# Kernel optimization log

Hardware: AMD Instinct MI355X
Metric: run time of the kernel (lower is better)

Reference implementation:

```python
import jax, jax.numpy as jnp
import numpy as np

N, E, P = 20000, 640000, 200000
IN_DIM, HID, HEADS, OUT_DIM = 256, 64, 4, 86
NEG_SLOPE = 0.2


def _gat_layer(h_in, src, dst, W, a_src, a_dst, b, heads, concat):
    n = h_in.shape[0]
    c = W.shape[1] // heads
    h = (h_in @ W).reshape(n, heads, c)                      # [N,H,C]
    alpha_s = jnp.sum(h * a_src, axis=-1)                    # [N,H]
    alpha_d = jnp.sum(h * a_dst, axis=-1)                    # [N,H]
    e = alpha_s[src] + alpha_d[dst]                          # [E,H]
    e = jnp.where(e > 0, e, NEG_SLOPE * e)                   # leaky_relu(0.2)
    # softmax over incoming edges of each destination node
    m = jax.ops.segment_max(e, dst, num_segments=n)          # [N,H]
    e = jnp.exp(e - m[dst])
    denom = jax.ops.segment_sum(e, dst, num_segments=n)      # [N,H]
    w = e / denom[dst]                                       # [E,H]
    msg = h[src] * w[:, :, None]                             # [E,H,C]
    out = jax.ops.segment_sum(msg, dst, num_segments=n)      # [N,H,C]
    if concat:
        out = out.reshape(n, heads * c)
    else:
        out = out.mean(axis=1)
    return out + b


def setup_inputs() -> dict:
    key = jax.random.key(0)
    ks = jax.random.split(key, 16)
    s = lambda *d: 1.0 / np.sqrt(d[0])
    x = jax.random.normal(ks[0], (N, IN_DIM), jnp.float32)
    edge_index = jax.random.randint(ks[1], (2, E), 0, N, jnp.int32)
    drug_pairs = jax.random.randint(ks[2], (P, 2), 0, N, jnp.int32)
    W1 = jax.random.normal(ks[3], (IN_DIM, HEADS * HID), jnp.float32) * s(IN_DIM)
    a_src1 = jax.random.normal(ks[4], (HEADS, HID), jnp.float32) * s(HID)
    a_dst1 = jax.random.normal(ks[5], (HEADS, HID), jnp.float32) * s(HID)
    b1 = jnp.zeros((HEADS * HID,), jnp.float32)
    W2 = jax.random.normal(ks[6], (HEADS * HID, HID), jnp.float32) * s(HEADS * HID)
    a_src2 = jax.random.normal(ks[7], (1, HID), jnp.float32) * s(HID)
    a_dst2 = jax.random.normal(ks[8], (1, HID), jnp.float32) * s(HID)
    b2 = jnp.zeros((HID,), jnp.float32)
    Wp1 = jax.random.normal(ks[9], (2 * HID, HID), jnp.float32) * s(2 * HID)
    bp1 = jnp.zeros((HID,), jnp.float32)
    Wp2 = jax.random.normal(ks[10], (HID, OUT_DIM), jnp.float32) * s(HID)
    bp2 = jnp.zeros((OUT_DIM,), jnp.float32)
    return dict(x=x, edge_index=edge_index, drug_pairs=drug_pairs,
                W1=W1, a_src1=a_src1, a_dst1=a_dst1, b1=b1,
                W2=W2, a_src2=a_src2, a_dst2=a_dst2, b2=b2,
                Wp1=Wp1, bp1=bp1, Wp2=Wp2, bp2=bp2)


def reference(x, edge_index, drug_pairs, W1, a_src1, a_dst1, b1,
              W2, a_src2, a_dst2, b2, Wp1, bp1, Wp2, bp2):
    n = x.shape[0]
    # PyG GATConv default add_self_loops=True
    loop = jnp.arange(n, dtype=edge_index.dtype)
    src = jnp.concatenate([edge_index[0], loop])
    dst = jnp.concatenate([edge_index[1], loop])
    h = _gat_layer(x, src, dst, W1, a_src1, a_dst1, b1, HEADS, concat=True)
    h = jax.nn.elu(h)  # dropout is identity in eval mode
    h = _gat_layer(h, src, dst, W2, a_src2, a_dst2, b2, 1, concat=False)
    h = jax.nn.elu(h)
    combined = jnp.concatenate([h[drug_pairs[:, 0]], h[drug_pairs[:, 1]]], axis=1)
    z = jax.nn.relu(combined @ Wp1 + bp1)
    return z @ Wp2 + bp2
```

## Files before the change

### kernel.cpp

```cpp
#include <hip/hip_runtime.h>
#include <hip/hip_fp16.h>

#define NN 20000
#define NE 640000
#define NEE 660000
#define NP 200000
#define NEG 0.2f

typedef _Float16 f16;
typedef __attribute__((ext_vector_type(4))) _Float16 f16x4;
typedef __attribute__((ext_vector_type(8))) _Float16 f16x8;
typedef __attribute__((ext_vector_type(4))) float f32x4;

__global__ void k_hist(const int* __restrict__ ei, int* __restrict__ cnt) {
  int i = blockIdx.x * 256 + threadIdx.x;
  if (i >= NEE) return;
  int d = (i < NE) ? ei[NE + i] : (i - NE);
  atomicAdd(&cnt[d], 1);
}

__global__ __launch_bounds__(1024) void k_scan(const int* __restrict__ cnt, int* __restrict__ rp) {
  __shared__ int ps[1024];
  const int CH = 20;
  int t = threadIdx.x;
  int lo = t * CH, hi = lo + CH;
  if (hi > NN) hi = NN;
  if (lo > NN) lo = NN;
  int s = 0;
  for (int i = lo; i < hi; ++i) s += cnt[i];
  ps[t] = s;
  __syncthreads();
  for (int off = 1; off < 1024; off <<= 1) {
    int v = (t >= off) ? ps[t - off] : 0;
    __syncthreads();
    ps[t] += v;
    __syncthreads();
  }
  int run = (t > 0) ? ps[t - 1] : 0;
  for (int i = lo; i < hi; ++i) { rp[i] = run; run += cnt[i]; }
  if (t == 1023) rp[NN] = ps[1023];
}

__global__ void k_scatter(const int* __restrict__ ei, const int* __restrict__ rp,
                          int* __restrict__ cur, int* __restrict__ col) {
  int i = blockIdx.x * 256 + threadIdx.x;
  if (i >= NEE) return;
  int s, d;
  if (i < NE) { s = ei[i]; d = ei[NE + i]; } else { s = i - NE; d = s; }
  int pos = atomicAdd(&cur[d], 1);
  col[rp[d] + pos] = s;
}

__global__ void k_cvt(const float* __restrict__ x, const float* __restrict__ W1,
                      f16* __restrict__ xh, f16* __restrict__ W1T) {
  int i = blockIdx.x * 256 + threadIdx.x;
  if (i < NN * 256 / 4) {
    float4 v = ((const float4*)x)[i];
    f16x4 h; h.x = (f16)v.x; h.y = (f16)v.y; h.z = (f16)v.z; h.w = (f16)v.w;
    *(f16x4*)(xh + (size_t)i * 4) = h;
  } else {
    int j = i - NN * 256 / 4;
    if (j < 256 * 256) {
      int r = j >> 8, c = j & 255;
      W1T[c * 256 + r] = (f16)W1[j];
    }
  }
}

__global__ void k_prep(const float* __restrict__ Wp2, const float* __restrict__ bp2,
                       const float* __restrict__ W2,
                       f16* __restrict__ Wp2Th, float* __restrict__ bp2p,
                       f16* __restrict__ W2T) {
  int i = blockIdx.x * 256 + threadIdx.x;
  if (i < 96 * 64) {
    int o = i >> 6, t = i & 63;
    Wp2Th[o * 64 + t] = (o < 86) ? (f16)Wp2[t * 86 + o] : (f16)0.f;
  }
  if (i < 96) bp2p[i] = (i < 86) ? bp2[i] : 0.f;
  if (i < 64 * 256) {
    int n = i >> 8, k = i & 255;
    W2T[n * 256 + k] = (f16)W2[k * 64 + n];
  }
}

__global__ __launch_bounds__(256) void k_gemm1(
    const f16* __restrict__ xh, const f16* __restrict__ W1T,
    const float* __restrict__ as1, const float* __restrict__ ad1,
    __half* __restrict__ h1h16, float* __restrict__ AS1, float* __restrict__ AD1) {
  __shared__ f16 xs[16][264];
  int tid = threadIdx.x;
  int base = blockIdx.x * 16;
  {
    int r = tid >> 4, ch = tid & 15;
    const uint4* src = (const uint4*)(xh + (size_t)(base + r) * 256 + ch * 16);
    uint4 v0 = src[0], v1 = src[1];
    *(uint4*)&xs[r][ch * 16] = v0;
    *(uint4*)&xs[r][ch * 16 + 8] = v1;
  }
  __syncthreads();
  int wv = tid >> 6, lane = tid & 63;
  int head = wv;
  int lr = lane & 15, lk = lane >> 4;
  f32x4 acc[4] = {{0.f,0.f,0.f,0.f},{0.f,0.f,0.f,0.f},{0.f,0.f,0.f,0.f},{0.f,0.f,0.f,0.f}};
#pragma unroll
  for (int k0 = 0; k0 < 256; k0 += 32) {
    f16x8 a = *(const f16x8*)&xs[lr][k0 + lk * 8];
#pragma unroll
    for (int nt = 0; nt < 4; ++nt) {
      int n = head * 64 + nt * 16 + lr;
      f16x8 b = *(const f16x8*)(W1T + (size_t)n * 256 + k0 + lk * 8);
      acc[nt] = __builtin_amdgcn_mfma_f32_16x16x32_f16(a, b, acc[nt], 0, 0, 0);
    }
  }
#pragma unroll
  for (int nt = 0; nt < 4; ++nt) {
    int cc = nt * 16 + lr;
#pragma unroll
    for (int r = 0; r < 4; ++r) {
      int row = lk * 4 + r;
      h1h16[((size_t)head * NN + base + row) * 64 + cc] = __float2half(acc[nt][r]);
    }
  }
#pragma unroll
  for (int r = 0; r < 4; ++r) {
    float ps = 0.f, pd = 0.f;
#pragma unroll
    for (int nt = 0; nt < 4; ++nt) {
      int cc = nt * 16 + lr;
      ps += acc[nt][r] * as1[head * 64 + cc];
      pd += acc[nt][r] * ad1[head * 64 + cc];
    }
#pragma unroll
    for (int off = 1; off < 16; off <<= 1) {
      ps += __shfl_xor(ps, off);
      pd += __shfl_xor(pd, off);
    }
    if (lr == 0) {
      int n = base + lk * 4 + r;
      AS1[n * 4 + head] = ps;
      AD1[n * 4 + head] = pd;
    }
  }
}

__global__ __launch_bounds__(256, 4) void k_agg1(
    const int* __restrict__ rp, const int* __restrict__ col,
    const float* __restrict__ AS1, const float* __restrict__ AD1,
    const __half* __restrict__ h1h16, const float* __restrict__ b1,
    __half* __restrict__ out16) {
  int b = blockIdx.x;
  int xcd = b & 7;
  int head = xcd >> 1;
  int grp = (b >> 3) * 2 + (xcd & 1);
  int wave = threadIdx.x >> 6, lane = threadIdx.x & 63;
  int n = grp * 4 + wave;
  int g = lane >> 3, c8 = (lane & 7) * 8;
  int e0 = rp[n], e1 = rp[n + 1];
  const __half* hs = h1h16 + (size_t)head * NN * 64;
  float adv = AD1[n * 4 + head];
  float acc[8] = {0.f,0.f,0.f,0.f,0.f,0.f,0.f,0.f};
  float den = 0.f;

  int ee = e0 + g;
  bool v = ee < e1;
  int ec = v ? ee : e1 - 1;
  int s = col[ec];
  float asv = AS1[s * 4 + head];

  for (int e = e0; e < e1; e += 8) {
    int een = e + 8 + g;
    bool vn = een < e1;
    int ecn = vn ? een : e1 - 1;
    int sn = col[ecn];
    float asn = AS1[sn * 4 + head];
    float ev = asv + adv;
    ev = fmaxf(ev, NEG * ev);
    float p = v ? __expf(ev) : 0.f;
    float4 raw = *(const float4*)(hs + (size_t)s * 64 + c8);
    const __half2* hp = (const __half2*)&raw;
#pragma unroll
    for (int m = 0; m < 4; ++m) {
      float2 f = __half22float2(hp[m]);
      acc[m * 2]     += p * f.x;
      acc[m * 2 + 1] += p * f.y;
    }
    den += p;
    s = sn; asv = asn; v = vn;
  }
#pragma unroll
  for (int i = 0; i < 8; ++i) {
    acc[i] += __shfl_xor(acc[i], 8);
    acc[i] += __shfl_xor(acc[i], 16);
    acc[i] += __shfl_xor(acc[i], 32);
  }
  den += __shfl_xor(den, 8); den += __shfl_xor(den, 16); den += __shfl_xor(den, 32);
  if (lane < 8) {
    float inv = 1.f / den;
    int cbase = head * 64 + lane * 8;
    __half ho[8];
#pragma unroll
    for (int i = 0; i < 8; ++i) {
      float r = acc[i] * inv + b1[cbase + i];
      r = r > 0.f ? r : __expf(r) - 1.f;
      ho[i] = __float2half(r);
    }
    *(uint4*)(out16 + (size_t)n * 256 + cbase) = *(uint4*)&ho[0];
  }
}

__global__ __launch_bounds__(256) void k_gemm2(
    const f16* __restrict__ h1a16, const f16* __restrict__ W2T,
    const float* __restrict__ as2, const float* __restrict__ ad2,
    __half* __restrict__ h2h16, float* __restrict__ AS2, float* __restrict__ AD2) {
  __shared__ f16 xs[16][264];
  __shared__ float psL[4][16], pdL[4][16];
  int tid = threadIdx.x;
  int base = blockIdx.x * 16;
  {
    int r = tid >> 4, ch = tid & 15;
    const uint4* src = (const uint4*)(h1a16 + (size_t)(base + r) * 256 + ch * 16);
    uint4 v0 = src[0], v1 = src[1];
    *(uint4*)&xs[r][ch * 16] = v0;
    *(uint4*)&xs[r][ch * 16 + 8] = v1;
  }
  __syncthreads();
  int wv = tid >> 6, lane = tid & 63;
  int lr = lane & 15, lk = lane >> 4;
  f32x4 acc = {0.f, 0.f, 0.f, 0.f};
#pragma unroll
  for (int k0 = 0; k0 < 256; k0 += 32) {
    f16x8 a = *(const f16x8*)&xs[lr][k0 + lk * 8];
    f16x8 b = *(const f16x8*)(W2T + (size_t)(wv * 16 + lr) * 256 + k0 + lk * 8);
    acc = __builtin_amdgcn_mfma_f32_16x16x32_f16(a, b, acc, 0, 0, 0);
  }
  int cc = wv * 16 + lr;
  float asv = as2[cc], adv = ad2[cc];
  float psr[4], pdr[4];
#pragma unroll
  for (int r = 0; r < 4; ++r) {
    int row = lk * 4 + r;
    h2h16[(size_t)(base + row) * 64 + cc] = __float2half(acc[r]);
    float ps = acc[r] * asv, pd = acc[r] * adv;
#pragma unroll
    for (int off = 1; off < 16; off <<= 1) {
      ps += __shfl_xor(ps, off);
      pd += __shfl_xor(pd, off);
    }
    psr[r] = ps; pdr[r] = pd;
  }
  if (lr == 0) {
#pragma unroll
    for (int r = 0; r < 4; ++r) {
      psL[wv][lk * 4 + r] = psr[r];
      pdL[wv][lk * 4 + r] = pdr[r];
    }
  }
  __syncthreads();
  if (tid < 16) {
    AS2[base + tid] = psL[0][tid] + psL[1][tid] + psL[2][tid] + psL[3][tid];
    AD2[base + tid] = pdL[0][tid] + pdL[1][tid] + pdL[2][tid] + pdL[3][tid];
  }
}

__global__ __launch_bounds__(256, 4) void k_agg2(
    const int* __restrict__ rp, const int* __restrict__ col,
    const float* __restrict__ AS2, const float* __restrict__ AD2,
    const __half* __restrict__ h2h16, const float* __restrict__ b2,
    float* __restrict__ out) {
  int wave = threadIdx.x >> 6, lane = threadIdx.x & 63;
  int n = blockIdx.x * 4 + wave;
  int g = lane >> 3, c8 = (lane & 7) * 8;
  int e0 = rp[n], e1 = rp[n + 1];
  float adv = AD2[n];
  float acc[8] = {0.f,0.f,0.f,0.f,0.f,0.f,0.f,0.f};
  float den = 0.f;

  int ee = e0 + g;
  bool v = ee < e1;
  int ec = v ? ee : e1 - 1;
  int s = col[ec];
  float asv = AS2[s];

  for (int e = e0; e < e1; e += 8) {
    int een = e + 8 + g;
    bool vn = een < e1;
    int ecn = vn ? een : e1 - 1;
    int sn = col[ecn];
    float asn = AS2[sn];
    float ev = asv + adv;
    ev = fmaxf(ev, NEG * ev);
    float p = v ? __expf(ev) : 0.f;
    float4 raw = *(const float4*)(h2h16 + (size_t)s * 64 + c8);
    const __half2* hp = (const __half2*)&raw;
#pragma unroll
    for (int m = 0; m < 4; ++m) {
      float2 f = __half22float2(hp[m]);
      acc[m * 2]     += p * f.x;
      acc[m * 2 + 1] += p * f.y;
    }
    den += p;
    s = sn; asv = asn; v = vn;
  }
#pragma unroll
  for (int i = 0; i < 8; ++i) {
    acc[i] += __shfl_xor(acc[i], 8);
    acc[i] += __shfl_xor(acc[i], 16);
    acc[i] += __shfl_xor(acc[i], 32);
  }
  den += __shfl_xor(den, 8); den += __shfl_xor(den, 16); den += __shfl_xor(den, 32);
  if (lane < 8) {
    float inv = 1.f / den;
    int cbase = lane * 8;
    float o[8];
#pragma unroll
    for (int i = 0; i < 8; ++i) {
      float r = acc[i] * inv + b2[cbase + i];
      o[i] = r > 0.f ? r : __expf(r) - 1.f;
    }
    *(float4*)(out + (size_t)n * 64 + cbase) = *(float4*)&o[0];
    *(float4*)(out + (size_t)n * 64 + cbase + 4) = *(float4*)&o[4];
  }
}

__global__ __launch_bounds__(128) void k_predot(
    const float* __restrict__ h2a, const float* __restrict__ Wp1,
    const float* __restrict__ bp1, float* __restrict__ AB) {
  __shared__ float xsT[64][20];
  int c = threadIdx.x;
  int base = blockIdx.x * 16;
  for (int i = threadIdx.x; i < 16 * 64; i += 128) {
    int r = i >> 6, k = i & 63;
    xsT[k][r] = h2a[(size_t)(base + r) * 64 + k];
  }
  __syncthreads();
  int part = c >> 6, u = c & 63;
  float bv = (part == 0) ? bp1[u] : 0.f;
  float acc[16];
#pragma unroll
  for (int r = 0; r < 16; ++r) acc[r] = bv;
#pragma unroll 2
  for (int k = 0; k < 64; ++k) {
    float wv = Wp1[(size_t)(part * 64 + k) * 64 + u];
    const float4* xr = (const float4*)&xsT[k][0];
    float4 x0 = xr[0], x1 = xr[1], x2 = xr[2], x3 = xr[3];
    acc[0] += x0.x * wv; acc[1] += x0.y * wv; acc[2] += x0.z * wv; acc[3] += x0.w * wv;
    acc[4] += x1.x * wv; acc[5] += x1.y * wv; acc[6] += x1.z * wv; acc[7] += x1.w * wv;
    acc[8] += x2.x * wv; acc[9] += x2.y * wv; acc[10] += x2.z * wv; acc[11] += x2.w * wv;
    acc[12] += x3.x * wv; acc[13] += x3.y * wv; acc[14] += x3.z * wv; acc[15] += x3.w * wv;
  }
#pragma unroll
  for (int r = 0; r < 16; ++r) AB[(size_t)(base + r) * 128 + c] = acc[r];
}

__global__ __launch_bounds__(256) void k_pairs(
    const int* __restrict__ pairs, const float* __restrict__ AB,
    const f16* __restrict__ Wp2Th, const float* __restrict__ bp2p,
    float* __restrict__ out) {
  __shared__ f16 zh[64][72];
  int tid = threadIdx.x;
  int pp = tid & 63, q = tid >> 6;
  int p = blockIdx.x * 64 + pp;
  int pi = pairs[2 * p], pj = pairs[2 * p + 1];

  {
    const float4* ar = (const float4*)(AB + (size_t)pi * 128 + q * 16);
    const float4* br = (const float4*)(AB + (size_t)pj * 128 + 64 + q * 16);
    f16 zv[16];
#pragma unroll
    for (int m = 0; m < 4; ++m) {
      float4 a = ar[m], b = br[m];
      zv[m * 4]     = (f16)fmaxf(a.x + b.x, 0.f);
      zv[m * 4 + 1] = (f16)fmaxf(a.y + b.y, 0.f);
      zv[m * 4 + 2] = (f16)fmaxf(a.z + b.z, 0.f);
      zv[m * 4 + 3] = (f16)fmaxf(a.w + b.w, 0.f);
    }
    *(uint4*)&zh[pp][q * 16] = *(uint4*)&zv[0];
    *(uint4*)&zh[pp][q * 16 + 8] = *(uint4*)&zv[8];
  }
  __syncthreads();

  int wv = tid >> 6, lane = tid & 63;
  int lr = lane & 15, lk = lane >> 4;
#pragma unroll
  for (int nt = 0; nt < 6; ++nt) {
    f32x4 acc = {0.f, 0.f, 0.f, 0.f};
#pragma unroll
    for (int k0 = 0; k0 < 64; k0 += 32) {
      f16x8 a = *(const f16x8*)&zh[wv * 16 + lr][k0 + lk * 8];
      f16x8 b = *(const f16x8*)(Wp2Th + (size_t)(nt * 16 + lr) * 64 + k0 + lk * 8);
      acc = __builtin_amdgcn_mfma_f32_16x16x32_f16(a, b, acc, 0, 0, 0);
    }
    int o = nt * 16 + lr;
    if (o < 86) {
      float bb = bp2p[o];
#pragma unroll
      for (int r = 0; r < 4; ++r) {
        int pr = blockIdx.x * 64 + wv * 16 + lk * 4 + r;
        out[(size_t)pr * 86 + o] = acc[r] + bb;
      }
    }
  }
}

extern "C" void kernel_launch(void* const* d_in, const int* in_sizes, int n_in,
                              void* d_out, int out_size, void* d_ws, size_t ws_size,
                              hipStream_t stream) {
  (void)in_sizes; (void)n_in; (void)out_size; (void)ws_size;
  const float* x      = (const float*)d_in[0];
  const int*   ei     = (const int*)d_in[1];
  const int*   pairs  = (const int*)d_in[2];
  const float* W1     = (const float*)d_in[3];
  const float* a_src1 = (const float*)d_in[4];
  const float* a_dst1 = (const float*)d_in[5];
  const float* b1     = (const float*)d_in[6];
  const float* W2     = (const float*)d_in[7];
  const float* a_src2 = (const float*)d_in[8];
  const float* a_dst2 = (const float*)d_in[9];
  const float* b2     = (const float*)d_in[10];
  const float* Wp1    = (const float*)d_in[11];
  const float* bp1    = (const float*)d_in[12];
  const float* Wp2    = (const float*)d_in[13];
  const float* bp2    = (const float*)d_in[14];
  float* out = (float*)d_out;

  char* w = (char*)d_ws;
  auto alloc = [&](size_t bytes) -> void* {
    void* pp = (void*)w;
    w += (bytes + 255) & ~(size_t)255;
    return pp;
  };
  __half* h1h16 = (__half*)alloc((size_t)NN * 256 * 2);
  float*  AS1   = (float*)alloc((size_t)NN * 4 * 4);
  float*  AD1   = (float*)alloc((size_t)NN * 4 * 4);
  __half* h1a16 = (__half*)alloc((size_t)NN * 256 * 2);
  __half* h2h16 = (__half*)alloc((size_t)NN * 64 * 2);
  float*  AS2   = (float*)alloc((size_t)NN * 4);
  float*  AD2   = (float*)alloc((size_t)NN * 4);
  float*  h2agg = (float*)alloc((size_t)NN * 64 * 4);
  float*  AB    = (float*)alloc((size_t)NN * 128 * 4);
  f16*    xh    = (f16*)alloc((size_t)NN * 256 * 2);
  f16*    W1T   = (f16*)alloc((size_t)256 * 256 * 2);
  f16*    Wp2Th = (f16*)alloc((size_t)96 * 64 * 2);
  float*  bp2p  = (float*)alloc(96 * 4);
  f16*    W2T   = (f16*)alloc((size_t)64 * 256 * 2);
  int*    rp    = (int*)alloc((size_t)(NN + 1) * 4);
  int*    cnt   = (int*)alloc((size_t)NN * 4);
  int*    cur   = (int*)alloc((size_t)NN * 4);
  int*    col   = (int*)alloc((size_t)NEE * 4);

  (void)hipMemsetAsync(cnt, 0, (size_t)NN * 4, stream);
  (void)hipMemsetAsync(cur, 0, (size_t)NN * 4, stream);

  const int EB = (NEE + 255) / 256;
  k_hist<<<EB, 256, 0, stream>>>(ei, cnt);
  k_scan<<<1, 1024, 0, stream>>>(cnt, rp);
  k_scatter<<<EB, 256, 0, stream>>>(ei, rp, cur, col);
  k_cvt<<<NN * 256 / 4 / 256 + 256, 256, 0, stream>>>(x, W1, xh, W1T);
  k_prep<<<64, 256, 0, stream>>>(Wp2, bp2, W2, Wp2Th, bp2p, W2T);

  k_gemm1<<<NN / 16, 256, 0, stream>>>(xh, W1T, a_src1, a_dst1, h1h16, AS1, AD1);
  k_agg1<<<NN, 256, 0, stream>>>(rp, col, AS1, AD1, h1h16, b1, h1a16);

  k_gemm2<<<NN / 16, 256, 0, stream>>>((const f16*)h1a16, W2T, a_src2, a_dst2, h2h16, AS2, AD2);
  k_agg2<<<NN / 4, 256, 0, stream>>>(rp, col, AS2, AD2, h2h16, b2, h2agg);

  k_predot<<<NN / 16, 128, 0, stream>>>(h2agg, Wp1, bp1, AB);
  k_pairs<<<NP / 64, 256, 0, stream>>>(pairs, AB, Wp2Th, bp2p, out);
}
```

Baseline: 267.6 us.

## Precompute per-edge attention weights in separate kernels and fuse x conversion into gemm1

Adds k_edgew1/k_edgew2 kernels that compute leaky-relu'd exponentiated attention scores per CSR edge (using a new dst array written during scatter), so the aggregation kernels stream contiguous weights instead of gathering AS[src] and computing exp per edge. It also removes the separate fp32->fp16 conversion kernel for x by converting inside gemm1's shared-memory load, and moves the W1 transpose into k_prep. The trade-off is extra launches and extra global traffic for the dst array and the weight buffers (4*NEE floats for layer 1), in exchange for fewer random gathers and less work in the aggregation loops.

```diff
diff --git a/kernel.cpp b/kernel.cpp
--- a/kernel.cpp
+++ b/kernel.cpp
@@ -42,35 +42,21 @@
 }
 
 __global__ void k_scatter(const int* __restrict__ ei, const int* __restrict__ rp,
-                          int* __restrict__ cur, int* __restrict__ col) {
+                          int* __restrict__ cur, int* __restrict__ col,
+                          int* __restrict__ dstv) {
   int i = blockIdx.x * 256 + threadIdx.x;
   if (i >= NEE) return;
   int s, d;
   if (i < NE) { s = ei[i]; d = ei[NE + i]; } else { s = i - NE; d = s; }
   int pos = atomicAdd(&cur[d], 1);
   col[rp[d] + pos] = s;
-}
-
-__global__ void k_cvt(const float* __restrict__ x, const float* __restrict__ W1,
-                      f16* __restrict__ xh, f16* __restrict__ W1T) {
-  int i = blockIdx.x * 256 + threadIdx.x;
-  if (i < NN * 256 / 4) {
-    float4 v = ((const float4*)x)[i];
-    f16x4 h; h.x = (f16)v.x; h.y = (f16)v.y; h.z = (f16)v.z; h.w = (f16)v.w;
-    *(f16x4*)(xh + (size_t)i * 4) = h;
-  } else {
-    int j = i - NN * 256 / 4;
-    if (j < 256 * 256) {
-      int r = j >> 8, c = j & 255;
-      W1T[c * 256 + r] = (f16)W1[j];
-    }
-  }
+  dstv[rp[d] + pos] = d;
 }
 
 __global__ void k_prep(const float* __restrict__ Wp2, const float* __restrict__ bp2,
-                       const float* __restrict__ W2,
+                       const float* __restrict__ W2, const float* __restrict__ W1,
                        f16* __restrict__ Wp2Th, float* __restrict__ bp2p,
-                       f16* __restrict__ W2T) {
+                       f16* __restrict__ W2T, f16* __restrict__ W1T) {
   int i = blockIdx.x * 256 + threadIdx.x;
   if (i < 96 * 64) {
     int o = i >> 6, t = i & 63;
@@ -81,10 +67,14 @@
     int n = i >> 8, k = i & 255;
     W2T[n * 256 + k] = (f16)W2[k * 64 + n];
   }
+  if (i < 256 * 256) {
+    int r = i >> 8, c = i & 255;
+    W1T[c * 256 + r] = (f16)W1[i];
+  }
 }
 
 __global__ __launch_bounds__(256) void k_gemm1(
-    const f16* __restrict__ xh, const f16* __restrict__ W1T,
+    const float* __restrict__ x, const f16* __restrict__ W1T,
     const float* __restrict__ as1, const float* __restrict__ ad1,
     __half* __restrict__ h1h16, float* __restrict__ AS1, float* __restrict__ AD1) {
   __shared__ f16 xs[16][264];
@@ -92,10 +82,15 @@
   int base = blockIdx.x * 16;
   {
     int r = tid >> 4, ch = tid & 15;
-    const uint4* src = (const uint4*)(xh + (size_t)(base + r) * 256 + ch * 16);
-    uint4 v0 = src[0], v1 = src[1];
-    *(uint4*)&xs[r][ch * 16] = v0;
-    *(uint4*)&xs[r][ch * 16 + 8] = v1;
+    const float4* src = (const float4*)(x + (size_t)(base + r) * 256 + ch * 16);
+    float4 a0 = src[0], a1 = src[1], a2 = src[2], a3 = src[3];
+    f16 tmp[16];
+    tmp[0] = (f16)a0.x; tmp[1] = (f16)a0.y; tmp[2] = (f16)a0.z; tmp[3] = (f16)a0.w;
+    tmp[4] = (f16)a1.x; tmp[5] = (f16)a1.y; tmp[6] = (f16)a1.z; tmp[7] = (f16)a1.w;
+    tmp[8] = (f16)a2.x; tmp[9] = (f16)a2.y; tmp[10] = (f16)a2.z; tmp[11] = (f16)a2.w;
+    tmp[12] = (f16)a3.x; tmp[13] = (f16)a3.y; tmp[14] = (f16)a3.z; tmp[15] = (f16)a3.w;
+    *(uint4*)&xs[r][ch * 16] = *(uint4*)&tmp[0];
+    *(uint4*)&xs[r][ch * 16 + 8] = *(uint4*)&tmp[8];
   }
   __syncthreads();
   int wv = tid >> 6, lane = tid & 63;
@@ -143,11 +138,29 @@
   }
 }
 
+__global__ void k_edgew1(const int* __restrict__ col, const int* __restrict__ dstv,
+                         const float* __restrict__ AS1, const float* __restrict__ AD1,
+                         float* __restrict__ w1) {
+  int i = blockIdx.x * 256 + threadIdx.x;
+  if (i >= NEE) return;
+  int s = col[i], d = dstv[i];
+  float4 as = *(const float4*)(AS1 + s * 4);
+  float4 ad = *(const float4*)(AD1 + d * 4);
+  float e0 = as.x + ad.x, e1 = as.y + ad.y, e2 = as.z + ad.z, e3 = as.w + ad.w;
+  e0 = fmaxf(e0, NEG * e0);
+  e1 = fmaxf(e1, NEG * e1);
+  e2 = fmaxf(e2, NEG * e2);
+  e3 = fmaxf(e3, NEG * e3);
+  w1[0 * NEE + i] = __expf(e0);
+  w1[1 * NEE + i] = __expf(e1);
+  w1[2 * NEE + i] = __expf(e2);
+  w1[3 * NEE + i] = __expf(e3);
+}
+
 __global__ __launch_bounds__(256, 4) void k_agg1(
     const int* __restrict__ rp, const int* __restrict__ col,
-    const float* __restrict__ AS1, const float* __restrict__ AD1,
-    const __half* __restrict__ h1h16, const float* __restrict__ b1,
-    __half* __restrict__ out16) {
+    const float* __restrict__ w1, const __half* __restrict__ h1h16,
+    const float* __restrict__ b1, __half* __restrict__ out16) {
   int b = blockIdx.x;
   int xcd = b & 7;
   int head = xcd >> 1;
@@ -157,7 +170,7 @@
   int g = lane >> 3, c8 = (lane & 7) * 8;
   int e0 = rp[n], e1 = rp[n + 1];
   const __half* hs = h1h16 + (size_t)head * NN * 64;
-  float adv = AD1[n * 4 + head];
+  const float* wp = w1 + (size_t)head * NEE;
   float acc[8] = {0.f,0.f,0.f,0.f,0.f,0.f,0.f,0.f};
   float den = 0.f;
 
@@ -165,27 +178,20 @@
   bool v = ee < e1;
   int ec = v ? ee : e1 - 1;
   int s = col[ec];
-  float asv = AS1[s * 4 + head];
+  float pw = v ? wp[ec] : 0.f;
 
   for (int e = e0; e < e1; e += 8) {
     int een = e + 8 + g;
     bool vn = een < e1;
     int ecn = vn ? een : e1 - 1;
     int sn = col[ecn];
-    float asn = AS1[sn * 4 + head];
-    float ev = asv + adv;
-    ev = fmaxf(ev, NEG * ev);
-    float p = v ? __expf(ev) : 0.f;
+    float pwn = vn ? wp[ecn] : 0.f;
     float4 raw = *(const float4*)(hs + (size_t)s * 64 + c8);
-    const __half2* hp = (const __half2*)&raw;
-#pragma unroll
-    for (int m = 0; m < 4; ++m) {
-      float2 f = __half22float2(hp[m]);
-      acc[m * 2]     += p * f.x;
-      acc[m * 2 + 1] += p * f.y;
-    }
-    den += p;
-    s = sn; asv = asn; v = vn;
+    const f16* hf = (const f16*)&raw;
+#pragma unroll
+    for (int i = 0; i < 8; ++i) acc[i] += pw * (float)hf[i];
+    den += pw;
+    s = sn; pw = pwn;
   }
 #pragma unroll
   for (int i = 0; i < 8; ++i) {
@@ -262,16 +268,25 @@
   }
 }
 
+__global__ void k_edgew2(const int* __restrict__ col, const int* __restrict__ dstv,
+                         const float* __restrict__ AS2, const float* __restrict__ AD2,
+                         float* __restrict__ w2) {
+  int i = blockIdx.x * 256 + threadIdx.x;
+  if (i >= NEE) return;
+  int s = col[i], d = dstv[i];
+  float ev = AS2[s] + AD2[d];
+  ev = fmaxf(ev, NEG * ev);
+  w2[i] = __expf(ev);
+}
+
 __global__ __launch_bounds__(256, 4) void k_agg2(
     const int* __restrict__ rp, const int* __restrict__ col,
-    const float* __restrict__ AS2, const float* __restrict__ AD2,
-    const __half* __restrict__ h2h16, const float* __restrict__ b2,
-    float* __restrict__ out) {
+    const float* __restrict__ w2, const __half* __restrict__ h2h16,
+    const float* __restrict__ b2, float* __restrict__ out) {
   int wave = threadIdx.x >> 6, lane = threadIdx.x & 63;
   int n = blockIdx.x * 4 + wave;
   int g = lane >> 3, c8 = (lane & 7) * 8;
   int e0 = rp[n], e1 = rp[n + 1];
-  float adv = AD2[n];
   float acc[8] = {0.f,0.f,0.f,0.f,0.f,0.f,0.f,0.f};
   float den = 0.f;
 
@@ -279,27 +294,20 @@
   bool v = ee < e1;
   int ec = v ? ee : e1 - 1;
   int s = col[ec];
-  float asv = AS2[s];
+  float pw = v ? w2[ec] : 0.f;
 
   for (int e = e0; e < e1; e += 8) {
     int een = e + 8 + g;
     bool vn = een < e1;
     int ecn = vn ? een : e1 - 1;
     int sn = col[ecn];
-    float asn = AS2[sn];
-    float ev = asv + adv;
-    ev = fmaxf(ev, NEG * ev);
-    float p = v ? __expf(ev) : 0.f;
+    float pwn = vn ? w2[ecn] : 0.f;
     float4 raw = *(const float4*)(h2h16 + (size_t)s * 64 + c8);
-    const __half2* hp = (const __half2*)&raw;
-#pragma unroll
-    for (int m = 0; m < 4; ++m) {
-      float2 f = __half22float2(hp[m]);
-      acc[m * 2]     += p * f.x;
-      acc[m * 2 + 1] += p * f.y;
-    }
-    den += p;
-    s = sn; asv = asn; v = vn;
+    const f16* hf = (const f16*)&raw;
+#pragma unroll
+    for (int i = 0; i < 8; ++i) acc[i] += pw * (float)hf[i];
+    den += pw;
+    s = sn; pw = pwn;
   }
 #pragma unroll
   for (int i = 0; i < 8; ++i) {
@@ -438,15 +446,17 @@
   float*  AD2   = (float*)alloc((size_t)NN * 4);
   float*  h2agg = (float*)alloc((size_t)NN * 64 * 4);
   float*  AB    = (float*)alloc((size_t)NN * 128 * 4);
-  f16*    xh    = (f16*)alloc((size_t)NN * 256 * 2);
   f16*    W1T   = (f16*)alloc((size_t)256 * 256 * 2);
   f16*    Wp2Th = (f16*)alloc((size_t)96 * 64 * 2);
   float*  bp2p  = (float*)alloc(96 * 4);
   f16*    W2T   = (f16*)alloc((size_t)64 * 256 * 2);
+  float*  w1    = (float*)alloc((size_t)4 * NEE * 4);
+  float*  w2    = (float*)alloc((size_t)NEE * 4);
   int*    rp    = (int*)alloc((size_t)(NN + 1) * 4);
   int*    cnt   = (int*)alloc((size_t)NN * 4);
   int*    cur   = (int*)alloc((size_t)NN * 4);
   int*    col   = (int*)alloc((size_t)NEE * 4);
+  int*    dstv  = (int*)alloc((size_t)NEE * 4);
 
   (void)hipMemsetAsync(cnt, 0, (size_t)NN * 4, stream);
   (void)hipMemsetAsync(cur, 0, (size_t)NN * 4, stream);
@@ -454,15 +464,16 @@
   const int EB = (NEE + 255) / 256;
   k_hist<<<EB, 256, 0, stream>>>(ei, cnt);
   k_scan<<<1, 1024, 0, stream>>>(cnt, rp);
-  k_scatter<<<EB, 256, 0, stream>>>(ei, rp, cur, col);
-  k_cvt<<<NN * 256 / 4 / 256 + 256, 256, 0, stream>>>(x, W1, xh, W1T);
-  k_prep<<<64, 256, 0, stream>>>(Wp2, bp2, W2, Wp2Th, bp2p, W2T);
-
-  k_gemm1<<<NN / 16, 256, 0, stream>>>(xh, W1T, a_src1, a_dst1, h1h16, AS1, AD1);
-  k_agg1<<<NN, 256, 0, stream>>>(rp, col, AS1, AD1, h1h16, b1, h1a16);
+  k_scatter<<<EB, 256, 0, stream>>>(ei, rp, cur, col, dstv);
+  k_prep<<<256, 256, 0, stream>>>(Wp2, bp2, W2, W1, Wp2Th, bp2p, W2T, W1T);
+
+  k_gemm1<<<NN / 16, 256, 0, stream>>>(x, W1T, a_src1, a_dst1, h1h16, AS1, AD1);
+  k_edgew1<<<EB, 256, 0, stream>>>(col, dstv, AS1, AD1, w1);
+  k_agg1<<<NN, 256, 0, stream>>>(rp, col, w1, h1h16, b1, h1a16);
 
   k_gemm2<<<NN / 16, 256, 0, stream>>>((const f16*)h1a16, W2T, a_src2, a_dst2, h2h16, AS2, AD2);
-  k_agg2<<<NN / 4, 256, 0, stream>>>(rp, col, AS2, AD2, h2h16, b2, h2agg);
+  k_edgew2<<<EB, 256, 0, stream>>>(col, dstv, AS2, AD2, w2);
+  k_agg2<<<NN / 4, 256, 0, stream>>>(rp, col, w2, h2h16, b2, h2agg);
 
   k_predot<<<NN / 16, 128, 0, stream>>>(h2agg, Wp1, bp1, AB);
   k_pairs<<<NP / 64, 256, 0, stream>>>(pairs, AB, Wp2Th, bp2p, out);
```

Result: slower. 275.9 us (+3.1%).
